# Optimization experiments

Measured on AMD Instinct MI355X. Metric: run time of the kernel, lower is better.

## Reference

```python
import jax, jax.numpy as jnp
import numpy as np

NUM_HEAD = 8
HIDDEN = 128
INPUT_DIM = 256
N1 = 1024
N2 = 1024
BATCH = 16


def setup_inputs() -> dict:
    key = jax.random.key(0)
    ks = jax.random.split(key, 10)
    HD = HIDDEN * NUM_HEAD  # 1024
    return {
        "x1": jax.random.normal(ks[0], (BATCH, N1, INPUT_DIM), jnp.float32),
        "x2": jax.random.normal(ks[1], (BATCH, N2, INPUT_DIM), jnp.float32),
        "B": jax.random.normal(ks[2], (N1, N2), jnp.float32),
        "wq_w": jax.random.normal(ks[3], (HD, INPUT_DIM), jnp.float32) * 0.02,
        "wq_b": jnp.zeros((HD,), jnp.float32),
        "wk_w": jax.random.normal(ks[4], (HD, INPUT_DIM), jnp.float32) * 0.02,
        "wk_b": jnp.zeros((HD,), jnp.float32),
        "wv_w": jax.random.normal(ks[5], (HD, INPUT_DIM), jnp.float32) * 0.02,
        "wv_b": jnp.zeros((HD,), jnp.float32),
        "proj_w": jax.random.normal(ks[6], (HIDDEN, HD), jnp.float32) * 0.02,
        "proj_b": jnp.zeros((HIDDEN,), jnp.float32),
    }


def reference(x1, x2, B, wq_w, wq_b, wk_w, wk_b, wv_w, wv_b, proj_w, proj_b):
    b, n1, _ = x1.shape
    n2 = x2.shape[1]
    sdk = jnp.sqrt(jnp.asarray(HIDDEN, x1.dtype))
    # Linear layers (torch convention: y = x @ W.T + b)
    q = x1 @ wq_w.T + wq_b                      # [b, n1, H*D]
    k = x2 @ wk_w.T + wk_b                      # [b, n2, H*D]
    v = x2 @ wv_w.T + wv_b                      # [b, n2, H*D]
    q = q.reshape(b, n1, NUM_HEAD, HIDDEN)
    k = k.reshape(b, n2, NUM_HEAD, HIDDEN)
    v = v.reshape(b, n2, NUM_HEAD, HIDDEN)
    # scores: [b, h, n1, n2]
    scores = jnp.einsum("bnhd,bmhd->bhnm", q, k) / sdk + B[None, None, :, :]
    attn = jax.nn.softmax(scores, axis=-1)
    out = jnp.einsum("bhnm,bmhd->bnhd", attn, v).reshape(b, n1, NUM_HEAD * HIDDEN)
    return out @ proj_w.T + proj_b              # [b, n1, HIDDEN]
```

## Files before the change

kernel.cpp:

```cpp
#include <hip/hip_runtime.h>
#include <hip/hip_fp16.h>

typedef _Float16 f16;
typedef __attribute__((ext_vector_type(4))) _Float16 f16x4;
typedef __attribute__((ext_vector_type(8))) _Float16 f16x8;
typedef __attribute__((ext_vector_type(4))) float f32x4;

#define MFMA_F16(a,b,c) __builtin_amdgcn_mfma_f32_16x16x32_f16((a),(b),(c),0,0,0)

__device__ __forceinline__ void gl_lds16(const f16* g, f16* l) {
  __builtin_amdgcn_global_load_lds(
      (const __attribute__((address_space(1))) unsigned int*)g,
      (__attribute__((address_space(3))) unsigned int*)l, 16, 0, 0);
}


__global__ __launch_bounds__(256) void gemm_qkv(
    const float* __restrict__ x1, const float* __restrict__ x2,
    const float* __restrict__ wq, const float* __restrict__ wqb,
    const float* __restrict__ wk, const float* __restrict__ wkb,
    const float* __restrict__ wv, const float* __restrict__ wvb,
    f16* __restrict__ Qp, f16* __restrict__ Kp, f16* __restrict__ Vp,
    float qscale) {
  constexpr int LD = 72;
  __shared__ f16 As[128][LD];
  __shared__ f16 Bs[128][LD];
  const int z = blockIdx.z;
  const float* X    = (z == 0) ? x1 : x2;
  const float* W    = (z == 0) ? wq : (z == 1) ? wk : wv;
  const float* bias = (z == 0) ? wqb : (z == 1) ? wkb : wvb;
  f16* outp         = (z == 0) ? Qp : (z == 1) ? Kp : Vp;
  const float sc    = (z == 0) ? qscale : 1.0f;

  const int tid = threadIdx.x, lane = tid & 63, wid = tid >> 6;
  const int col = lane & 15, quad = lane >> 4;
  const int wm = (wid >> 1) * 64, wn = (wid & 1) * 64;
  const int n0x = blockIdx.x * 128;
  const int m0w = blockIdx.y * 128;

  const int rr = tid >> 4, cc4 = tid & 15;

  f32x4 acc[4][4];
#pragma unroll
  for (int i = 0; i < 4; i++)
#pragma unroll
    for (int j = 0; j < 4; j++) acc[i][j] = (f32x4){0.f, 0.f, 0.f, 0.f};

  float4 wreg[8], xreg[8];
#pragma unroll
  for (int i = 0; i < 8; i++) {
    wreg[i] = *(const float4*)(W + (size_t)(m0w + rr + i * 16) * 256 + cc4 * 4);
    xreg[i] = *(const float4*)(X + (size_t)(n0x + rr + i * 16) * 256 + cc4 * 4);
  }

  for (int kt = 0; kt < 4; ++kt) {
#pragma unroll
    for (int i = 0; i < 8; i++) {
      float4 v = wreg[i];
      f16x4 hh; hh[0] = (f16)v.x; hh[1] = (f16)v.y; hh[2] = (f16)v.z; hh[3] = (f16)v.w;
      *(f16x4*)&As[rr + i * 16][cc4 * 4] = hh;
      v = xreg[i];
      f16x4 hg; hg[0] = (f16)v.x; hg[1] = (f16)v.y; hg[2] = (f16)v.z; hg[3] = (f16)v.w;
      *(f16x4*)&Bs[rr + i * 16][cc4 * 4] = hg;
    }
    __syncthreads();
    if (kt < 3) {
      const int k0 = (kt + 1) * 64;
#pragma unroll
      for (int i = 0; i < 8; i++) {
        wreg[i] = *(const float4*)(W + (size_t)(m0w + rr + i * 16) * 256 + k0 + cc4 * 4);
        xreg[i] = *(const float4*)(X + (size_t)(n0x + rr + i * 16) * 256 + k0 + cc4 * 4);
      }
    }
    const f16 (*Rs)[LD] = (z == 2) ? Bs : As;
    const f16 (*Cs)[LD] = (z == 2) ? As : Bs;
#pragma unroll
    for (int ks = 0; ks < 2; ks++) {
      f16x8 af[4], bf[4];
#pragma unroll
      for (int i = 0; i < 4; i++) af[i] = *(const f16x8*)&Rs[wm + i * 16 + col][ks * 32 + quad * 8];
#pragma unroll
      for (int j = 0; j < 4; j++) bf[j] = *(const f16x8*)&Cs[wn + j * 16 + col][ks * 32 + quad * 8];
#pragma unroll
      for (int i = 0; i < 4; i++)
#pragma unroll
        for (int j = 0; j < 4; j++) acc[i][j] = MFMA_F16(af[i], bf[j], acc[i][j]);
    }
    __syncthreads();
  }

  const int h = blockIdx.y;
  if (z < 2) {
#pragma unroll
    for (int i = 0; i < 4; i++) {
      const int k0h = wm + i * 16 + quad * 4;
      float4 bq = *(const float4*)(bias + h * 128 + k0h);
      const int ks2 = k0h >> 5, q2 = (k0h >> 3) & 3, lo = k0h & 7;
#pragma unroll
      for (int j = 0; j < 4; j++) {
        const int bn2 = n0x + wn + j * 16 + col;
        const int b = bn2 >> 10, n2 = bn2 & 1023;
        const int T = n2 >> 6, jt = (n2 >> 4) & 3, c2 = n2 & 15;
        f16x4 pk;
#pragma unroll
        for (int r = 0; r < 4; r++)
          pk[r] = (f16)((acc[i][j][r] + ((const float*)&bq)[r]) * sc);
        *(f16x4*)(outp + (size_t)(b * 8 + h) * 131072 + T * 8192 +
                  (jt * 4 + ks2) * 512 + (q2 * 16 + c2) * 8 + lo) = pk;
      }
    }
  } else {
#pragma unroll
    for (int j = 0; j < 4; j++) {
      const int d = wn + j * 16 + col;
      const float bv = bias[h * 128 + d];
      const int ct = d >> 4, c2 = d & 15;
#pragma unroll
      for (int i = 0; i < 4; i++) {
        const int bn2 = n0x + wm + i * 16 + quad * 4;
        const int b = bn2 >> 10, n2 = bn2 & 1023;
        const int T = n2 >> 6, kv0 = n2 & 63;
        const int ks2 = kv0 >> 5, q2 = (kv0 >> 3) & 3, lo = kv0 & 7;
        f16x4 pk;
#pragma unroll
        for (int r = 0; r < 4; r++) pk[r] = (f16)(acc[i][j][r] + bv);
        *(f16x4*)(outp + (size_t)(b * 8 + h) * 131072 + T * 8192 +
                  (ct * 2 + ks2) * 512 + (q2 * 16 + c2) * 8 + lo) = pk;
      }
    }
  }
}

__global__ __launch_bounds__(256) void gemm_proj(const f16* __restrict__ A,
                                                 const float* __restrict__ W,
                                                 const float* __restrict__ bias,
                                                 float* __restrict__ out) {
  constexpr int LD = 72;
  __shared__ f16 As[64][LD];
  __shared__ f16 Bs[64][LD];
  const int tid = threadIdx.x, lane = tid & 63, wid = tid >> 6;
  const int col = lane & 15, quad = lane >> 4;
  const int wm = (wid >> 1) * 32, wn = (wid & 1) * 32;
  const int m0 = blockIdx.x * 64, n0 = blockIdx.y * 64;

  f32x4 acc[2][2];
#pragma unroll
  for (int i = 0; i < 2; i++)
#pragma unroll
    for (int j = 0; j < 2; j++) acc[i][j] = (f32x4){0.f, 0.f, 0.f, 0.f};

  for (int kt = 0; kt < 16; ++kt) {
    const int k0 = kt * 64;
#pragma unroll
    for (int i = 0; i < 2; i++) {
      int f = i * 256 + tid;
      int r = f >> 3, ch = f & 7;
      *(f16x8*)&As[r][ch * 8] = *(const f16x8*)(A + (size_t)(m0 + r) * 1024 + k0 + ch * 8);
    }
#pragma unroll
    for (int i = 0; i < 4; i++) {
      int f = i * 256 + tid;
      int r = f >> 4, c4 = f & 15;
      float4 v = *(const float4*)(W + (size_t)(n0 + r) * 1024 + k0 + c4 * 4);
      f16x4 hh; hh[0] = (f16)v.x; hh[1] = (f16)v.y; hh[2] = (f16)v.z; hh[3] = (f16)v.w;
      *(f16x4*)&Bs[r][c4 * 4] = hh;
    }
    __syncthreads();
#pragma unroll
    for (int ks = 0; ks < 2; ks++) {
      f16x8 af[2], bf[2];
#pragma unroll
      for (int i = 0; i < 2; i++) af[i] = *(const f16x8*)&As[wm + i * 16 + col][ks * 32 + quad * 8];
#pragma unroll
      for (int j = 0; j < 2; j++) bf[j] = *(const f16x8*)&Bs[wn + j * 16 + col][ks * 32 + quad * 8];
#pragma unroll
      for (int i = 0; i < 2; i++)
#pragma unroll
        for (int j = 0; j < 2; j++) acc[i][j] = MFMA_F16(af[i], bf[j], acc[i][j]);
    }
    __syncthreads();
  }
#pragma unroll
  for (int j = 0; j < 2; j++) {
    const int c = n0 + wn + j * 16 + col;
    const float bv = bias[c];
#pragma unroll
    for (int i = 0; i < 2; i++) {
      const int r0 = m0 + wm + i * 16 + quad * 4;
#pragma unroll
      for (int r = 0; r < 4; r++)
        out[(size_t)(r0 + r) * 128 + c] = acc[i][j][r] + bv;
    }
  }
}

__global__ __launch_bounds__(512) __attribute__((amdgpu_waves_per_eu(4, 4)))
void attn_fused(const f16* __restrict__ Qp, const f16* __restrict__ Kp,
                const f16* __restrict__ Vp, const float* __restrict__ Bm,
                f16* __restrict__ O) {
  __shared__ f16 Ksl[2][8192];
  __shared__ f16 Vtl[2][8192];
  __shared__ f16 Ps[8192];
  const int tid = threadIdx.x, lane = tid & 63, wid = tid >> 6;
  const int col = lane & 15, quad = lane >> 4;
  const int id = blockIdx.x;
  const int mt = (id >> 3) & 7;
  const int bh = ((id >> 6) << 3) | (id & 7);
  const int b = bh >> 3, h = bh & 7;
  const int m0 = mt * 128;
  const int wm = wid * 16;

  const f16* Qb = Qp + (size_t)bh * 131072;
  const f16* Kb = Kp + (size_t)bh * 131072;
  const f16* Vb = Vp + (size_t)bh * 131072;

#define ISSUE(T, bufi)                                                        \
  {                                                                           \
    if (wid < 4) {                                                            \
      _Pragma("unroll") for (int j = 0; j < 4; j++)                           \
          gl_lds16(Kb + (size_t)(T) * 8192 + (wid * 4 + j) * 512 + lane * 8,  \
                   &Ksl[bufi][(wid * 4 + j) * 512]);                          \
    } else {                                                                  \
      _Pragma("unroll") for (int j = 0; j < 4; j++)                           \
          gl_lds16(Vb + (size_t)(T) * 8192 + ((wid - 4) * 4 + j) * 512 + lane * 8, \
                   &Vtl[bufi][((wid - 4) * 4 + j) * 512]);                    \
    }                                                                         \
  }

  ISSUE(0, 0);
  ISSUE(1, 1);

  f16x8 qf[4];
  {
    const int m = m0 + wm;
    const int T = m >> 6, jt2 = (m >> 4) & 3;
#pragma unroll
    for (int ks = 0; ks < 4; ks++)
      qf[ks] = *(const f16x8*)(Qb + T * 8192 + (jt2 * 4 + ks) * 512 + lane * 8);
  }

  f32x4 oacc[8];
  float l = 0.f;
#pragma unroll
  for (int ct = 0; ct < 8; ct++) oacc[ct] = (f32x4){0.f, 0.f, 0.f, 0.f};

  __syncthreads();

  for (int t = 0; t < 16; ++t) {
    const int buf = t & 1;
    const int n0 = t * 64;

    float4 breg[4];
    {
      const float* Brow = Bm + (size_t)(m0 + wm + col) * 1024 + n0;
#pragma unroll
      for (int jt = 0; jt < 4; jt++)
        breg[jt] = *(const float4*)(Brow + jt * 16 + quad * 4);
    }

    f32x4 s[4];
#pragma unroll
    for (int jt = 0; jt < 4; jt++) s[jt] = (f32x4){0.f, 0.f, 0.f, 0.f};
#pragma unroll
    for (int ks = 0; ks < 4; ks++) {
      f16x8 kf[4];
#pragma unroll
      for (int jt = 0; jt < 4; jt++)
        kf[jt] = *(const f16x8*)&Ksl[buf][(jt * 4 + ks) * 512 + lane * 8];
#pragma unroll
      for (int jt = 0; jt < 4; jt++) s[jt] = MFMA_F16(kf[jt], qf[ks], s[jt]);
    }

    {
      const int m = wm + col;
#pragma unroll
      for (int jt = 0; jt < 4; jt++) {
        const float* bv = (const float*)&breg[jt];
        float p0 = __expf(s[jt][0] + bv[0]);
        float p1 = __expf(s[jt][1] + bv[1]);
        float p2 = __expf(s[jt][2] + bv[2]);
        float p3 = __expf(s[jt][3] + bv[3]);
        l += (p0 + p1) + (p2 + p3);
        f16x4 pk; pk[0] = (f16)p0; pk[1] = (f16)p1; pk[2] = (f16)p2; pk[3] = (f16)p3;
        const int g = (jt * 2 + (quad >> 1)) ^ (col & 7);
        *(f16x4*)&Ps[m * 64 + g * 8 + (quad & 1) * 4] = pk;
      }
    }

#pragma unroll
    for (int ks = 0; ks < 2; ks++) {
      const int m = wm + col;
      const int g = (ks * 4 + quad) ^ (col & 7);
      f16x8 pf = *(const f16x8*)&Ps[m * 64 + g * 8];
#pragma unroll
      for (int ct = 0; ct < 8; ct++) {
        f16x8 vf = *(const f16x8*)&Vtl[buf][(ct * 2 + ks) * 512 + lane * 8];
        oacc[ct] = MFMA_F16(pf, vf, oacc[ct]);
      }
    }

    __syncthreads();
    if (t + 2 < 16) ISSUE(t + 2, buf);
  }

  l += __shfl_xor(l, 16);
  l += __shfl_xor(l, 32);
  f16* Ob = O + ((size_t)(b * 1024 + m0 + wm)) * 1024 + h * 128;
#pragma unroll
  for (int r = 0; r < 4; r++) {
    const float lv = __shfl(l, (lane & 48) | (quad * 4 + r));
    const float inv = 1.0f / lv;
#pragma unroll
    for (int ct = 0; ct < 8; ct++)
      Ob[(size_t)(quad * 4 + r) * 1024 + ct * 16 + col] = (f16)(oacc[ct][r] * inv);
  }
}

extern "C" void kernel_launch(void* const* d_in, const int* in_sizes, int n_in,
                              void* d_out, int out_size, void* d_ws, size_t ws_size,
                              hipStream_t stream) {
  (void)in_sizes; (void)n_in; (void)out_size; (void)ws_size;
  const float* x1  = (const float*)d_in[0];
  const float* x2  = (const float*)d_in[1];
  const float* Bm  = (const float*)d_in[2];
  const float* wq  = (const float*)d_in[3];
  const float* wqb = (const float*)d_in[4];
  const float* wk  = (const float*)d_in[5];
  const float* wkb = (const float*)d_in[6];
  const float* wv  = (const float*)d_in[7];
  const float* wvb = (const float*)d_in[8];
  const float* pw  = (const float*)d_in[9];
  const float* pb  = (const float*)d_in[10];
  float* out = (float*)d_out;

  const size_t ELEMS = (size_t)16 * 1024 * 1024;
  f16* Qp = (f16*)d_ws;
  f16* Kp = Qp + ELEMS;
  f16* Vp = Kp + ELEMS;
  f16* Ow = Vp + ELEMS;

  const float scale = 0.0883883476483184f;
  gemm_qkv<<<dim3(128, 8, 3), dim3(256), 0, stream>>>(x1, x2, wq, wqb, wk, wkb,
                                                      wv, wvb, Qp, Kp, Vp, scale);
  attn_fused<<<dim3(1024), dim3(512), 0, stream>>>(Qp, Kp, Vp, Bm, Ow);
  gemm_proj<<<dim3(256, 2), dim3(256), 0, stream>>>(Ow, pw, pb, out);
}
```

Before: 284.6 us.

## Switch attention to 32x32x16 MFMA with 4-wave blocks and retiled Q/K/V layout

Rewrites the fused attention kernel to use 32x32x16 MFMA tiles instead of 16x16x32. Each block now has 4 waves, each owning 32 query rows. The QKV projection epilogue writes Q, K and V in a new packed layout that matches the larger fragments, and the softmax, P staging and output writeback are remapped to the 32-lane fragment layout. The aim is fewer MFMA issues and LDS fragment loads per unit of work. In exchange each wave holds more accumulator registers and there are fewer waves per block to hide latency.

After: 301.5 us. 5.9% more time.

```diff
diff --git a/kernel.cpp b/kernel.cpp
--- a/kernel.cpp
+++ b/kernel.cpp
@@ -5,8 +5,10 @@
 typedef __attribute__((ext_vector_type(4))) _Float16 f16x4;
 typedef __attribute__((ext_vector_type(8))) _Float16 f16x8;
 typedef __attribute__((ext_vector_type(4))) float f32x4;
+typedef __attribute__((ext_vector_type(16))) float f32x16;
 
 #define MFMA_F16(a,b,c) __builtin_amdgcn_mfma_f32_16x16x32_f16((a),(b),(c),0,0,0)
+#define MFMA32(a,b,c)   __builtin_amdgcn_mfma_f32_32x32x16_f16((a),(b),(c),0,0,0)
 
 __device__ __forceinline__ void gl_lds16(const f16* g, f16* l) {
   __builtin_amdgcn_global_load_lds(
@@ -95,18 +97,18 @@
     for (int i = 0; i < 4; i++) {
       const int k0h = wm + i * 16 + quad * 4;
       float4 bq = *(const float4*)(bias + h * 128 + k0h);
-      const int ks2 = k0h >> 5, q2 = (k0h >> 3) & 3, lo = k0h & 7;
+      const int ks = k0h >> 4, jo = (k0h >> 3) & 1, off = k0h & 7;
 #pragma unroll
       for (int j = 0; j < 4; j++) {
         const int bn2 = n0x + wn + j * 16 + col;
         const int b = bn2 >> 10, n2 = bn2 & 1023;
-        const int T = n2 >> 6, jt = (n2 >> 4) & 3, c2 = n2 & 15;
+        const int T = n2 >> 6, jt = (n2 >> 5) & 1, lr = n2 & 31;
         f16x4 pk;
 #pragma unroll
         for (int r = 0; r < 4; r++)
           pk[r] = (f16)((acc[i][j][r] + ((const float*)&bq)[r]) * sc);
         *(f16x4*)(outp + (size_t)(b * 8 + h) * 131072 + T * 8192 +
-                  (jt * 4 + ks2) * 512 + (q2 * 16 + c2) * 8 + lo) = pk;
+                  (jt * 8 + ks) * 512 + (jo * 32 + lr) * 8 + off) = pk;
       }
     }
   } else {
@@ -114,18 +116,18 @@
     for (int j = 0; j < 4; j++) {
       const int d = wn + j * 16 + col;
       const float bv = bias[h * 128 + d];
-      const int ct = d >> 4, c2 = d & 15;
+      const int ct = d >> 5, lr = d & 31;
 #pragma unroll
       for (int i = 0; i < 4; i++) {
         const int bn2 = n0x + wm + i * 16 + quad * 4;
         const int b = bn2 >> 10, n2 = bn2 & 1023;
-        const int T = n2 >> 6, kv0 = n2 & 63;
-        const int ks2 = kv0 >> 5, q2 = (kv0 >> 3) & 3, lo = kv0 & 7;
+        const int T = n2 >> 6, kv6 = n2 & 63;
+        const int ks2 = kv6 >> 4, q2v = (kv6 >> 3) & 1, off = kv6 & 7;
         f16x4 pk;
 #pragma unroll
         for (int r = 0; r < 4; r++) pk[r] = (f16)(acc[i][j][r] + bv);
         *(f16x4*)(outp + (size_t)(b * 8 + h) * 131072 + T * 8192 +
-                  (ct * 2 + ks2) * 512 + (q2 * 16 + c2) * 8 + lo) = pk;
+                  (ct * 4 + ks2) * 512 + (q2v * 32 + lr) * 8 + off) = pk;
       }
     }
   }
@@ -194,7 +196,7 @@
   }
 }
 
-__global__ __launch_bounds__(512) __attribute__((amdgpu_waves_per_eu(4, 4)))
+__global__ __launch_bounds__(256) __attribute__((amdgpu_waves_per_eu(2, 2)))
 void attn_fused(const f16* __restrict__ Qp, const f16* __restrict__ Kp,
                 const f16* __restrict__ Vp, const float* __restrict__ Bm,
                 f16* __restrict__ O) {
@@ -202,47 +204,46 @@
   __shared__ f16 Vtl[2][8192];
   __shared__ f16 Ps[8192];
   const int tid = threadIdx.x, lane = tid & 63, wid = tid >> 6;
-  const int col = lane & 15, quad = lane >> 4;
+  const int lo5 = lane & 31, q2 = lane >> 5;
   const int id = blockIdx.x;
   const int mt = (id >> 3) & 7;
   const int bh = ((id >> 6) << 3) | (id & 7);
   const int b = bh >> 3, h = bh & 7;
   const int m0 = mt * 128;
-  const int wm = wid * 16;
+  const int wm = wid * 32;
 
   const f16* Qb = Qp + (size_t)bh * 131072;
   const f16* Kb = Kp + (size_t)bh * 131072;
   const f16* Vb = Vp + (size_t)bh * 131072;
 
-#define ISSUE(T, bufi)                                                        \
-  {                                                                           \
-    if (wid < 4) {                                                            \
-      _Pragma("unroll") for (int j = 0; j < 4; j++)                           \
-          gl_lds16(Kb + (size_t)(T) * 8192 + (wid * 4 + j) * 512 + lane * 8,  \
-                   &Ksl[bufi][(wid * 4 + j) * 512]);                          \
-    } else {                                                                  \
-      _Pragma("unroll") for (int j = 0; j < 4; j++)                           \
-          gl_lds16(Vb + (size_t)(T) * 8192 + ((wid - 4) * 4 + j) * 512 + lane * 8, \
-                   &Vtl[bufi][((wid - 4) * 4 + j) * 512]);                    \
-    }                                                                         \
+#define ISSUE(T, bufi)                                                       \
+  {                                                                          \
+    _Pragma("unroll") for (int j = 0; j < 4; j++) {                          \
+      gl_lds16(Kb + (size_t)(T) * 8192 + (wid * 4 + j) * 512 + lane * 8,     \
+               &Ksl[bufi][(wid * 4 + j) * 512]);                             \
+      gl_lds16(Vb + (size_t)(T) * 8192 + (wid * 4 + j) * 512 + lane * 8,     \
+               &Vtl[bufi][(wid * 4 + j) * 512]);                             \
+    }                                                                        \
   }
 
   ISSUE(0, 0);
   ISSUE(1, 1);
 
-  f16x8 qf[4];
+  f16x8 qf[8];
   {
     const int m = m0 + wm;
-    const int T = m >> 6, jt2 = (m >> 4) & 3;
-#pragma unroll
-    for (int ks = 0; ks < 4; ks++)
-      qf[ks] = *(const f16x8*)(Qb + T * 8192 + (jt2 * 4 + ks) * 512 + lane * 8);
-  }
-
-  f32x4 oacc[8];
+    const int T = m >> 6, jt = (m >> 5) & 1;
+#pragma unroll
+    for (int ks = 0; ks < 8; ks++)
+      qf[ks] = *(const f16x8*)(Qb + T * 8192 + (jt * 8 + ks) * 512 + lane * 8);
+  }
+
+  f32x16 oacc[4];
+#pragma unroll
+  for (int ct = 0; ct < 4; ct++)
+#pragma unroll
+    for (int r = 0; r < 16; r++) oacc[ct][r] = 0.f;
   float l = 0.f;
-#pragma unroll
-  for (int ct = 0; ct < 8; ct++) oacc[ct] = (f32x4){0.f, 0.f, 0.f, 0.f};
 
   __syncthreads();
 
@@ -250,69 +251,72 @@
     const int buf = t & 1;
     const int n0 = t * 64;
 
-    float4 breg[4];
+    float4 breg[2][4];
     {
-      const float* Brow = Bm + (size_t)(m0 + wm + col) * 1024 + n0;
-#pragma unroll
-      for (int jt = 0; jt < 4; jt++)
-        breg[jt] = *(const float4*)(Brow + jt * 16 + quad * 4);
-    }
-
-    f32x4 s[4];
-#pragma unroll
-    for (int jt = 0; jt < 4; jt++) s[jt] = (f32x4){0.f, 0.f, 0.f, 0.f};
-#pragma unroll
-    for (int ks = 0; ks < 4; ks++) {
-      f16x8 kf[4];
-#pragma unroll
-      for (int jt = 0; jt < 4; jt++)
-        kf[jt] = *(const f16x8*)&Ksl[buf][(jt * 4 + ks) * 512 + lane * 8];
-#pragma unroll
-      for (int jt = 0; jt < 4; jt++) s[jt] = MFMA_F16(kf[jt], qf[ks], s[jt]);
+      const float* Brow = Bm + (size_t)(m0 + wm + lo5) * 1024 + n0;
+#pragma unroll
+      for (int jt = 0; jt < 2; jt++)
+#pragma unroll
+        for (int zz = 0; zz < 4; zz++)
+          breg[jt][zz] = *(const float4*)(Brow + jt * 32 + zz * 8 + q2 * 4);
+    }
+
+    f32x16 sT[2];
+#pragma unroll
+    for (int jt = 0; jt < 2; jt++)
+#pragma unroll
+      for (int r = 0; r < 16; r++) sT[jt][r] = 0.f;
+#pragma unroll
+    for (int ks = 0; ks < 8; ks++) {
+      f16x8 kf0 = *(const f16x8*)&Ksl[buf][(0 * 8 + ks) * 512 + lane * 8];
+      f16x8 kf1 = *(const f16x8*)&Ksl[buf][(1 * 8 + ks) * 512 + lane * 8];
+      sT[0] = MFMA32(kf0, qf[ks], sT[0]);
+      sT[1] = MFMA32(kf1, qf[ks], sT[1]);
     }
 
     {
-      const int m = wm + col;
-#pragma unroll
-      for (int jt = 0; jt < 4; jt++) {
-        const float* bv = (const float*)&breg[jt];
-        float p0 = __expf(s[jt][0] + bv[0]);
-        float p1 = __expf(s[jt][1] + bv[1]);
-        float p2 = __expf(s[jt][2] + bv[2]);
-        float p3 = __expf(s[jt][3] + bv[3]);
-        l += (p0 + p1) + (p2 + p3);
-        f16x4 pk; pk[0] = (f16)p0; pk[1] = (f16)p1; pk[2] = (f16)p2; pk[3] = (f16)p3;
-        const int g = (jt * 2 + (quad >> 1)) ^ (col & 7);
-        *(f16x4*)&Ps[m * 64 + g * 8 + (quad & 1) * 4] = pk;
+      const int m = wm + lo5;
+#pragma unroll
+      for (int jt = 0; jt < 2; jt++)
+#pragma unroll
+        for (int zz = 0; zz < 4; zz++) {
+          const float* bv = (const float*)&breg[jt][zz];
+          float p0 = __expf(sT[jt][zz * 4 + 0] + bv[0]);
+          float p1 = __expf(sT[jt][zz * 4 + 1] + bv[1]);
+          float p2 = __expf(sT[jt][zz * 4 + 2] + bv[2]);
+          float p3 = __expf(sT[jt][zz * 4 + 3] + bv[3]);
+          l += (p0 + p1) + (p2 + p3);
+          f16x4 pk; pk[0] = (f16)p0; pk[1] = (f16)p1; pk[2] = (f16)p2; pk[3] = (f16)p3;
+          const int g = (jt * 4 + zz) ^ (m & 7);
+          *(f16x4*)&Ps[m * 64 + g * 8 + q2 * 4] = pk;
+        }
+    }
+
+#pragma unroll
+    for (int ks2 = 0; ks2 < 4; ks2++) {
+      const int m = wm + lo5;
+      const int g = (ks2 * 2 + q2) ^ (m & 7);
+      f16x8 pf = *(const f16x8*)&Ps[m * 64 + g * 8];
+#pragma unroll
+      for (int ct = 0; ct < 4; ct++) {
+        f16x8 vf = *(const f16x8*)&Vtl[buf][(ct * 4 + ks2) * 512 + lane * 8];
+        oacc[ct] = MFMA32(pf, vf, oacc[ct]);
       }
     }
 
-#pragma unroll
-    for (int ks = 0; ks < 2; ks++) {
-      const int m = wm + col;
-      const int g = (ks * 4 + quad) ^ (col & 7);
-      f16x8 pf = *(const f16x8*)&Ps[m * 64 + g * 8];
-#pragma unroll
-      for (int ct = 0; ct < 8; ct++) {
-        f16x8 vf = *(const f16x8*)&Vtl[buf][(ct * 2 + ks) * 512 + lane * 8];
-        oacc[ct] = MFMA_F16(pf, vf, oacc[ct]);
-      }
-    }
-
     __syncthreads();
     if (t + 2 < 16) ISSUE(t + 2, buf);
   }
 
-  l += __shfl_xor(l, 16);
   l += __shfl_xor(l, 32);
   f16* Ob = O + ((size_t)(b * 1024 + m0 + wm)) * 1024 + h * 128;
 #pragma unroll
-  for (int r = 0; r < 4; r++) {
-    const float lv = __shfl(l, (lane & 48) | (quad * 4 + r));
-    const float inv = 1.0f / lv;
-#pragma unroll
-    for (int ct = 0; ct < 8; ct++)
-      Ob[(size_t)(quad * 4 + r) * 1024 + ct * 16 + col] = (f16)(oacc[ct][r] * inv);
+  for (int r = 0; r < 16; r++) {
+    const int mloc = (r & 3) + 8 * (r >> 2) + 4 * q2;
+    const float inv = 1.0f / __shfl(l, mloc);
+#pragma unroll
+    for (int ct = 0; ct < 4; ct++)
+      Ob[(size_t)mloc * 1024 + ct * 32 + lo5] = (f16)(oacc[ct][r] * inv);
   }
 }
 
@@ -342,6 +346,6 @@
   const float scale = 0.0883883476483184f;
   gemm_qkv<<<dim3(128, 8, 3), dim3(256), 0, stream>>>(x1, x2, wq, wqb, wk, wkb,
                                                       wv, wvb, Qp, Kp, Vp, scale);
-  attn_fused<<<dim3(1024), dim3(512), 0, stream>>>(Qp, Kp, Vp, Bm, Ow);
+  attn_fused<<<dim3(1024), dim3(256), 0, stream>>>(Qp, Kp, Vp, Bm, Ow);
   gemm_proj<<<dim3(256, 2), dim3(256), 0, stream>>>(Ow, pw, pb, out);
 }
```

## Pre-pack inputs and weights to fp16 MFMA layout, stream QKV GEMM via LDS DMA

Applied to the files above, without the earlier changes.

Adds a conversion kernel that casts x1, x2 and the three weight matrices to fp16 once and stores them in MFMA-fragment order. The QKV GEMM then uses 512 threads with double-buffered global_load_lds, replacing the per-block fp32 loads and in-register conversion. This removes repeated conversion work and halves the bytes each GEMM block reads. In exchange it adds a kernel launch, an extra fp32 read plus fp16 write pass, and places the packed buffers in the workspace region that Ow later reuses.

Result: no change. 279.0 us (-2.0%).

```diff
diff --git a/kernel.cpp b/kernel.cpp
--- a/kernel.cpp
+++ b/kernel.cpp
@@ -15,90 +15,121 @@
 }
 
 
-__global__ __launch_bounds__(256) void gemm_qkv(
+__global__ __launch_bounds__(256) void conv_pack(
     const float* __restrict__ x1, const float* __restrict__ x2,
-    const float* __restrict__ wq, const float* __restrict__ wqb,
-    const float* __restrict__ wk, const float* __restrict__ wkb,
-    const float* __restrict__ wv, const float* __restrict__ wvb,
-    f16* __restrict__ Qp, f16* __restrict__ Kp, f16* __restrict__ Vp,
-    float qscale) {
-  constexpr int LD = 72;
-  __shared__ f16 As[128][LD];
-  __shared__ f16 Bs[128][LD];
+    const float* __restrict__ wq, const float* __restrict__ wk,
+    const float* __restrict__ wv,
+    f16* __restrict__ x1p, f16* __restrict__ x2p, f16* __restrict__ wp) {
+  __shared__ f16 S[128][264];
+  const int id = blockIdx.x, tid = threadIdx.x;
+  const float* src;
+  f16* dst;
+  if (id < 128) {
+    src = x1 + (size_t)id * 32768; dst = x1p + (size_t)id * 32768;
+  } else if (id < 256) {
+    src = x2 + (size_t)(id - 128) * 32768; dst = x2p + (size_t)(id - 128) * 32768;
+  } else {
+    const int wsel = (id - 256) >> 3, wt = (id - 256) & 7;
+    const float* wsrc = (wsel == 0) ? wq : (wsel == 1) ? wk : wv;
+    src = wsrc + (size_t)wt * 32768;
+    dst = wp + (size_t)wsel * 262144 + (size_t)wt * 32768;
+  }
+#pragma unroll 8
+  for (int i = 0; i < 32; i++) {
+    int f = i * 256 + tid;
+    int row = f >> 6, c4 = f & 63;
+    float4 v = *(const float4*)(src + (size_t)row * 256 + c4 * 4);
+    f16x4 hh; hh[0] = (f16)v.x; hh[1] = (f16)v.y; hh[2] = (f16)v.z; hh[3] = (f16)v.w;
+    *(f16x4*)&S[row][c4 * 4] = hh;
+  }
+  __syncthreads();
+#pragma unroll 8
+  for (int i = 0; i < 16; i++) {
+    int u = i * 256 + tid;
+    int chunk = u >> 6, l2 = u & 63;
+    int q = l2 >> 4, c = l2 & 15;
+    int row = (chunk >> 3) * 16 + c, k = (chunk & 7) * 32 + q * 8;
+    f16x8 v = *(const f16x8*)&S[row][k];
+    *(f16x8*)(dst + (size_t)u * 8) = v;
+  }
+}
+
+__global__ __launch_bounds__(512) __attribute__((amdgpu_waves_per_eu(4, 4)))
+void gemm_qkv(const f16* __restrict__ x1p, const f16* __restrict__ x2p,
+              const f16* __restrict__ wp,
+              const float* __restrict__ wqb, const float* __restrict__ wkb,
+              const float* __restrict__ wvb,
+              f16* __restrict__ Qp, f16* __restrict__ Kp, f16* __restrict__ Vp,
+              float qscale) {
+  __shared__ f16 Wl[2][8192];
+  __shared__ f16 Xl[2][8192];
   const int z = blockIdx.z;
-  const float* X    = (z == 0) ? x1 : x2;
-  const float* W    = (z == 0) ? wq : (z == 1) ? wk : wv;
+  const f16* Xp = (z == 0) ? x1p : x2p;
   const float* bias = (z == 0) ? wqb : (z == 1) ? wkb : wvb;
-  f16* outp         = (z == 0) ? Qp : (z == 1) ? Kp : Vp;
-  const float sc    = (z == 0) ? qscale : 1.0f;
+  f16* outp = (z == 0) ? Qp : (z == 1) ? Kp : Vp;
+  const float sc = (z == 0) ? qscale : 1.0f;
 
   const int tid = threadIdx.x, lane = tid & 63, wid = tid >> 6;
   const int col = lane & 15, quad = lane >> 4;
-  const int wm = (wid >> 1) * 64, wn = (wid & 1) * 64;
-  const int n0x = blockIdx.x * 128;
-  const int m0w = blockIdx.y * 128;
-
-  const int rr = tid >> 4, cc4 = tid & 15;
-
-  f32x4 acc[4][4];
+  const int xt = blockIdx.x, h = blockIdx.y;
+  const int wr = wid >> 2, xc = wid & 3;
+  const f16* Xb = Xp + (size_t)xt * 32768;
+  const f16* Wb = wp + (size_t)z * 262144 + (size_t)h * 32768;
+
+#define QISSUE(T, bufi)                                                   \
+  {                                                                       \
+    _Pragma("unroll") for (int j = 0; j < 2; j++) {                       \
+      int lc = wid * 2 + j;                                               \
+      int rt = lc >> 1, ksl = lc & 1;                                     \
+      gl_lds16(Wb + (size_t)((rt * 8 + (T) * 2 + ksl) << 9) + lane * 8,   \
+               &Wl[bufi][lc * 512]);                                      \
+      gl_lds16(Xb + (size_t)((rt * 8 + (T) * 2 + ksl) << 9) + lane * 8,   \
+               &Xl[bufi][lc * 512]);                                      \
+    }                                                                     \
+  }
+
+  QISSUE(0, 0);
+  QISSUE(1, 1);
+
+  f32x4 acc[4][2];
 #pragma unroll
   for (int i = 0; i < 4; i++)
 #pragma unroll
-    for (int j = 0; j < 4; j++) acc[i][j] = (f32x4){0.f, 0.f, 0.f, 0.f};
-
-  float4 wreg[8], xreg[8];
-#pragma unroll
-  for (int i = 0; i < 8; i++) {
-    wreg[i] = *(const float4*)(W + (size_t)(m0w + rr + i * 16) * 256 + cc4 * 4);
-    xreg[i] = *(const float4*)(X + (size_t)(n0x + rr + i * 16) * 256 + cc4 * 4);
-  }
-
-  for (int kt = 0; kt < 4; ++kt) {
-#pragma unroll
-    for (int i = 0; i < 8; i++) {
-      float4 v = wreg[i];
-      f16x4 hh; hh[0] = (f16)v.x; hh[1] = (f16)v.y; hh[2] = (f16)v.z; hh[3] = (f16)v.w;
-      *(f16x4*)&As[rr + i * 16][cc4 * 4] = hh;
-      v = xreg[i];
-      f16x4 hg; hg[0] = (f16)v.x; hg[1] = (f16)v.y; hg[2] = (f16)v.z; hg[3] = (f16)v.w;
-      *(f16x4*)&Bs[rr + i * 16][cc4 * 4] = hg;
+    for (int j = 0; j < 2; j++) acc[i][j] = (f32x4){0.f, 0.f, 0.f, 0.f};
+
+  __syncthreads();
+
+  for (int t = 0; t < 4; ++t) {
+    const int buf = t & 1;
+    const f16* Ra = (z == 2) ? Xl[buf] : Wl[buf];
+    const f16* Cb = (z == 2) ? Wl[buf] : Xl[buf];
+#pragma unroll
+    for (int ksl = 0; ksl < 2; ksl++) {
+      f16x8 af[4], bf[2];
+#pragma unroll
+      for (int i = 0; i < 4; i++)
+        af[i] = *(const f16x8*)&Ra[((wr * 4 + i) * 2 + ksl) * 512 + lane * 8];
+#pragma unroll
+      for (int j = 0; j < 2; j++)
+        bf[j] = *(const f16x8*)&Cb[((xc * 2 + j) * 2 + ksl) * 512 + lane * 8];
+#pragma unroll
+      for (int i = 0; i < 4; i++)
+#pragma unroll
+        for (int j = 0; j < 2; j++) acc[i][j] = MFMA_F16(af[i], bf[j], acc[i][j]);
     }
     __syncthreads();
-    if (kt < 3) {
-      const int k0 = (kt + 1) * 64;
-#pragma unroll
-      for (int i = 0; i < 8; i++) {
-        wreg[i] = *(const float4*)(W + (size_t)(m0w + rr + i * 16) * 256 + k0 + cc4 * 4);
-        xreg[i] = *(const float4*)(X + (size_t)(n0x + rr + i * 16) * 256 + k0 + cc4 * 4);
-      }
-    }
-    const f16 (*Rs)[LD] = (z == 2) ? Bs : As;
-    const f16 (*Cs)[LD] = (z == 2) ? As : Bs;
-#pragma unroll
-    for (int ks = 0; ks < 2; ks++) {
-      f16x8 af[4], bf[4];
-#pragma unroll
-      for (int i = 0; i < 4; i++) af[i] = *(const f16x8*)&Rs[wm + i * 16 + col][ks * 32 + quad * 8];
-#pragma unroll
-      for (int j = 0; j < 4; j++) bf[j] = *(const f16x8*)&Cs[wn + j * 16 + col][ks * 32 + quad * 8];
-#pragma unroll
-      for (int i = 0; i < 4; i++)
-#pragma unroll
-        for (int j = 0; j < 4; j++) acc[i][j] = MFMA_F16(af[i], bf[j], acc[i][j]);
-    }
-    __syncthreads();
-  }
-
-  const int h = blockIdx.y;
+    if (t + 2 < 4) QISSUE(t + 2, buf);
+  }
+
   if (z < 2) {
 #pragma unroll
     for (int i = 0; i < 4; i++) {
-      const int k0h = wm + i * 16 + quad * 4;
+      const int k0h = wr * 64 + i * 16 + quad * 4;
       float4 bq = *(const float4*)(bias + h * 128 + k0h);
       const int ks2 = k0h >> 5, q2 = (k0h >> 3) & 3, lo = k0h & 7;
 #pragma unroll
-      for (int j = 0; j < 4; j++) {
-        const int bn2 = n0x + wn + j * 16 + col;
+      for (int j = 0; j < 2; j++) {
+        const int bn2 = xt * 128 + xc * 32 + j * 16 + col;
         const int b = bn2 >> 10, n2 = bn2 & 1023;
         const int T = n2 >> 6, jt = (n2 >> 4) & 3, c2 = n2 & 15;
         f16x4 pk;
@@ -111,21 +142,21 @@
     }
   } else {
 #pragma unroll
-    for (int j = 0; j < 4; j++) {
-      const int d = wn + j * 16 + col;
+    for (int j = 0; j < 2; j++) {
+      const int d = xc * 32 + j * 16 + col;
       const float bv = bias[h * 128 + d];
-      const int ct = d >> 4, c2 = d & 15;
+      const int ct = d >> 4, cc = d & 15;
 #pragma unroll
       for (int i = 0; i < 4; i++) {
-        const int bn2 = n0x + wm + i * 16 + quad * 4;
+        const int bn2 = xt * 128 + wr * 64 + i * 16 + quad * 4;
         const int b = bn2 >> 10, n2 = bn2 & 1023;
-        const int T = n2 >> 6, kv0 = n2 & 63;
-        const int ks2 = kv0 >> 5, q2 = (kv0 >> 3) & 3, lo = kv0 & 7;
+        const int T = n2 >> 6, kv6 = n2 & 63;
+        const int ks2 = kv6 >> 5, qv = (kv6 >> 3) & 3, jj = kv6 & 7;
         f16x4 pk;
 #pragma unroll
         for (int r = 0; r < 4; r++) pk[r] = (f16)(acc[i][j][r] + bv);
         *(f16x4*)(outp + (size_t)(b * 8 + h) * 131072 + T * 8192 +
-                  (ct * 2 + ks2) * 512 + (q2 * 16 + c2) * 8 + lo) = pk;
+                  (ct * 2 + ks2) * 512 + (qv * 16 + cc) * 8 + jj) = pk;
       }
     }
   }
@@ -214,7 +245,7 @@
   const f16* Kb = Kp + (size_t)bh * 131072;
   const f16* Vb = Vp + (size_t)bh * 131072;
 
-#define ISSUE(T, bufi)                                                        \
+#define AISSUE(T, bufi)                                                       \
   {                                                                           \
     if (wid < 4) {                                                            \
       _Pragma("unroll") for (int j = 0; j < 4; j++)                           \
@@ -227,8 +258,8 @@
     }                                                                         \
   }
 
-  ISSUE(0, 0);
-  ISSUE(1, 1);
+  AISSUE(0, 0);
+  AISSUE(1, 1);
 
   f16x8 qf[4];
   {
@@ -300,7 +331,7 @@
     }
 
     __syncthreads();
-    if (t + 2 < 16) ISSUE(t + 2, buf);
+    if (t + 2 < 16) AISSUE(t + 2, buf);
   }
 
   l += __shfl_xor(l, 16);
@@ -333,15 +364,19 @@
   const float* pb  = (const float*)d_in[10];
   float* out = (float*)d_out;
 
-  const size_t ELEMS = (size_t)16 * 1024 * 1024;
-  f16* Qp = (f16*)d_ws;
-  f16* Kp = Qp + ELEMS;
-  f16* Vp = Kp + ELEMS;
-  f16* Ow = Vp + ELEMS;
+  const size_t MiB = 1024 * 1024;
+  f16* Qp  = (f16*)d_ws;
+  f16* Kp  = (f16*)((char*)d_ws + 32 * MiB);
+  f16* Vp  = (f16*)((char*)d_ws + 64 * MiB);
+  f16* Ow  = (f16*)((char*)d_ws + 96 * MiB);
+  f16* x1p = (f16*)((char*)d_ws + 96 * MiB);
+  f16* x2p = (f16*)((char*)d_ws + 104 * MiB);
+  f16* wp  = (f16*)((char*)d_ws + 112 * MiB);
 
   const float scale = 0.0883883476483184f;
-  gemm_qkv<<<dim3(128, 8, 3), dim3(256), 0, stream>>>(x1, x2, wq, wqb, wk, wkb,
-                                                      wv, wvb, Qp, Kp, Vp, scale);
+  conv_pack<<<dim3(280), dim3(256), 0, stream>>>(x1, x2, wq, wk, wv, x1p, x2p, wp);
+  gemm_qkv<<<dim3(128, 8, 3), dim3(512), 0, stream>>>(x1p, x2p, wp, wqb, wkb, wvb,
+                                                      Qp, Kp, Vp, scale);
   attn_fused<<<dim3(1024), dim3(512), 0, stream>>>(Qp, Kp, Vp, Bm, Ow);
   gemm_proj<<<dim3(256, 2), dim3(256), 0, stream>>>(Ow, pw, pb, out);
 }
```
